# Performance work log

Hardware: AMD Instinct MI355X
Metric: run time of the kernel (lower is better)

The kernel has to match this reference:

```python
import jax, jax.numpy as jnp
import numpy as np

B, V, C, H, W, D = 1, 3, 64, 96, 96, 48


def bilinear_sample(feat, gx, gy):
    """torch F.grid_sample(mode='bilinear', padding_mode='zeros', align_corners=True).
    feat: (B, C, H, W); gx, gy: (B, N) normalized coords in [-1, 1]. Returns (B, C, N)."""
    Bf, Cf, Hf, Wf = feat.shape
    x = (gx + 1.0) * 0.5 * (Wf - 1)
    y = (gy + 1.0) * 0.5 * (Hf - 1)
    x0 = jnp.floor(x)
    y0 = jnp.floor(y)
    wx1 = x - x0
    wy1 = y - y0
    wx0 = 1.0 - wx1
    wy0 = 1.0 - wy1
    flat = feat.reshape(Bf, Cf, Hf * Wf)

    def gather(xi, yi):
        valid = (xi >= 0) & (xi <= Wf - 1) & (yi >= 0) & (yi <= Hf - 1)
        xi_c = jnp.clip(xi, 0, Wf - 1).astype(jnp.int32)
        yi_c = jnp.clip(yi, 0, Hf - 1).astype(jnp.int32)
        idx = (yi_c * Wf + xi_c)[:, None, :]  # (B,1,N), broadcast over C
        return jnp.take_along_axis(flat, idx, axis=2) * valid[:, None, :]

    out = (gather(x0, y0) * (wx0 * wy0)[:, None]
           + gather(x0 + 1, y0) * (wx1 * wy0)[:, None]
           + gather(x0, y0 + 1) * (wx0 * wy1)[:, None]
           + gather(x0 + 1, y0 + 1) * (wx1 * wy1)[:, None])
    return out


def src_grid(proj_mat, depth_values, Hs, Ws):
    """homo_warp grid computation. proj_mat: (B,3,4); depth_values: (B,D).
    Returns normalized gx, gy each of shape (B, D*Hs*Ws)."""
    xs = jnp.arange(Ws, dtype=jnp.float32)
    ys = jnp.arange(Hs, dtype=jnp.float32)
    gx_, gy_ = jnp.meshgrid(xs, ys)  # (Hs, Ws) each
    ref = jnp.stack([gx_.ravel(), gy_.ravel(), jnp.ones(Hs * Ws, jnp.float32)], 0)  # (3, HW)
    R = proj_mat[:, :, :3]
    T = proj_mat[:, :, 3]
    # (B,3,D,HW): R @ p + T / depth
    pts = jnp.einsum('bij,jn->bin', R, ref)[:, :, None, :] + T[:, :, None, None] / depth_values[:, None, :, None]
    xy = pts[:, :2] / pts[:, 2:3]
    gx = xy[:, 0] / ((Ws - 1) / 2.0) - 1.0
    gy = xy[:, 1] / ((Hs - 1) / 2.0) - 1.0
    Bb = proj_mat.shape[0]
    return gx.reshape(Bb, -1), gy.reshape(Bb, -1)


def setup_inputs() -> dict:
    key = jax.random.key(0)
    k1, k2, k3, k4 = jax.random.split(key, 4)
    imgs = jax.random.normal(k1, (B, V, 3, H, W), jnp.float32)
    feats = jax.random.normal(k2, (B, V, C, H, W), jnp.float32)
    # near-identity projections so warped coords land mostly in-range (z ~ 1)
    eye = jnp.broadcast_to(jnp.eye(3, dtype=jnp.float32), (B, V, 3, 3))
    Rn = eye + 0.05 * jax.random.normal(k3, (B, V, 3, 3), jnp.float32)
    Tn = 0.5 * jax.random.normal(jax.random.fold_in(k3, 1), (B, V, 3, 1), jnp.float32)
    proj_mats = jnp.concatenate([Rn, Tn], axis=-1)
    depth_values = 2.0 + 4.0 * jax.random.uniform(k4, (B, D), jnp.float32)
    return {"imgs": imgs, "feats": feats, "proj_mats": proj_mats, "depth_values": depth_values}


def reference(imgs, feats, proj_mats, depth_values):
    Bb, Vv, _, Hh, Ww = imgs.shape
    Cc = feats.shape[2]
    Dd = depth_values.shape[1]
    # ref view volume (broadcast over D)
    ref_volume = jnp.broadcast_to(feats[:, 0][:, :, None], (Bb, Cc, Dd, Hh, Ww))
    volume_sum = ref_volume
    volume_sq_sum = ref_volume ** 2
    mask_sum = jnp.ones((Bb, Dd, Hh, Ww), jnp.float32)  # ref view always in-range
    img_chans = [jnp.broadcast_to(imgs[:, 0][:, :, None], (Bb, 3, Dd, Hh, Ww))]
    for i in range(Vv - 1):  # small fixed number of source views
        gx, gy = src_grid(proj_mats[:, i + 1], depth_values, Hh, Ww)
        wv = bilinear_sample(feats[:, i + 1], gx, gy).reshape(Bb, Cc, Dd, Hh, Ww)
        wi = bilinear_sample(imgs[:, i + 1], gx, gy).reshape(Bb, 3, Dd, Hh, Ww)
        m = ((gx > -1.0) & (gx < 1.0) & (gy > -1.0) & (gy < 1.0)).astype(jnp.float32).reshape(Bb, Dd, Hh, Ww)
        volume_sum = volume_sum + wv
        volume_sq_sum = volume_sq_sum + wv ** 2
        mask_sum = mask_sum + m
        img_chans.append(wi)
    count = 1.0 / mask_sum[:, None]  # (B,1,D,H,W)
    var = volume_sq_sum * count - (volume_sum * count) ** 2  # (B,C,D,H,W)
    img_chans.append(var)
    return jnp.concatenate(img_chans, axis=1)  # (B, 3*V + C, D, H, W)
```

## Files before the change

kernel.cpp:

```cpp
#include <hip/hip_runtime.h>

#define BDIM 256

constexpr int Vv = 3, Cc = 64, Hh = 96, Ww = 96, Dd = 48;
constexpr int HW = Hh * Ww;
constexpr int NPIX = Dd * HW;
constexpr int DHW = Dd * HW;
constexpr int NXCD = 8;
constexpr int WP = Ww + 4;

__device__ __forceinline__ void compute_warp_v(const float* __restrict__ P, float depth,
                                               float xf, float yf,
                                               int offs[4], float wts[4], float& inbf)
{
#pragma clang fp contract(off)
    const float r00 = P[0], r01 = P[1], r02 = P[2],  t0 = P[3];
    const float r10 = P[4], r11 = P[5], r12 = P[6],  t1 = P[7];
    const float r20 = P[8], r21 = P[9], r22 = P[10], t2 = P[11];

    const float px = ((r00 * xf + r01 * yf) + r02) + t0 / depth;
    const float py = ((r10 * xf + r11 * yf) + r12) + t1 / depth;
    const float pz = ((r20 * xf + r21 * yf) + r22) + t2 / depth;

    const float xy0 = px / pz;
    const float xy1 = py / pz;
    const float gx = xy0 / ((float)(Ww - 1) * 0.5f) - 1.0f;
    const float gy = xy1 / ((float)(Hh - 1) * 0.5f) - 1.0f;

    const bool inb = (gx > -1.0f) && (gx < 1.0f) && (gy > -1.0f) && (gy < 1.0f);
    inbf = inb ? 1.0f : 0.0f;

    const float sx = (gx + 1.0f) * 0.5f * (float)(Ww - 1);
    const float sy = (gy + 1.0f) * 0.5f * (float)(Hh - 1);
    const float x0 = floorf(sx), y0 = floorf(sy);
    const float wx1 = sx - x0, wy1 = sy - y0;
    const float wx0 = 1.0f - wx1, wy0 = 1.0f - wy1;

#pragma unroll
    for (int k = 0; k < 4; ++k) {
        const float xi = (k & 1) ? (x0 + 1.0f) : x0;
        const float yi = (k & 2) ? (y0 + 1.0f) : y0;
        const float wk = ((k & 1) ? wx1 : wx0) * ((k & 2) ? wy1 : wy0);
        const bool valid = (xi >= 0.0f) && (xi <= (float)(Ww - 1)) &&
                           (yi >= 0.0f) && (yi <= (float)(Hh - 1));
        const float xc = fminf(fmaxf(xi, 0.0f), (float)(Ww - 1));
        const float yc = fminf(fmaxf(yi, 0.0f), (float)(Hh - 1));
        offs[k] = (int)yc * Ww + (int)xc;
        wts[k] = valid ? wk : 0.0f;
    }
}

__device__ __forceinline__ void compute_warp(const float* __restrict__ proj, float depth,
                                             float xf, float yf,
                                             int offs[2][4], float wts[2][4], float& msum)
{
    msum = 1.0f;
#pragma unroll
    for (int v = 0; v < 2; ++v) {
        float inb;
        compute_warp_v(proj + (v + 1) * 12, depth, xf, yf, offs[v], wts[v], inb);
        msum += inb;
    }
}

__device__ __forceinline__ float var_one(float fr, float a1, float a2, float cnt)
{
    const float s  = fr + a1 + a2;
    const float q  = fr * fr + a1 * a1 + a2 * a2;
    const float sc = s * cnt;
    return q * cnt - sc * sc;
}

__global__ void __launch_bounds__(BDIM) transpose_feats_kernel(const float* __restrict__ feats,
                                                               float* __restrict__ ft)
{
    __shared__ float tile[64][65];
    const int v  = blockIdx.y;
    const int p0 = blockIdx.x * 64;
    const float* src = feats + (size_t)v * Cc * HW;

    const int px = threadIdx.x & 63;
    const int c0 = threadIdx.x >> 6;
#pragma unroll
    for (int c = c0; c < Cc; c += 4)
        tile[c][px] = src[(size_t)c * HW + p0 + px];
    __syncthreads();

    const int cc  = threadIdx.x & 63;
    const int pr0 = threadIdx.x >> 6;
    float* dst = ft + ((size_t)v * HW + p0) * Cc;
#pragma unroll
    for (int p = pr0; p < 64; p += 4)
        dst[p * Cc + cc] = tile[cc][p];
}

__global__ void __launch_bounds__(BDIM) ge_row_kernel(
    const float* __restrict__ imgs, const float* __restrict__ ftr,
    const float* __restrict__ proj, const float* __restrict__ depthv,
    float* __restrict__ out)
{
    __shared__ alignas(16) float s_tile[2][Cc / 2][WP];
    __shared__ alignas(16) int   s_base[2][2][Ww][4];
    __shared__ alignas(16) float s_wt[2][2][Ww][4];
    __shared__ float s_inb[2][2][Ww];

    const int nper = (Hh * (Dd / 2)) / NXCD;
    const int blk  = (blockIdx.x & (NXCD - 1)) * nper + (blockIdx.x >> 3);
    const int h   = blk / (Dd / 2);
    const int dq  = blk - h * (Dd / 2);
    const int d0  = dq * 2;
    const int tid = threadIdx.x;
    const int rowb0 = d0 * HW + h * Ww;

    if (tid < 2 * Ww) {
        const int v = (tid >= Ww) ? 1 : 0;
        const int w = tid - v * Ww;
        const float* ib = imgs + (size_t)(v + 1) * 3 * HW;
#pragma unroll
        for (int dd = 0; dd < 2; ++dd) {
            int offs[4];
            float wts[4];
            float inb;
            compute_warp_v(proj + (v + 1) * 12, depthv[d0 + dd], (float)w, (float)h,
                           offs, wts, inb);
            s_inb[v][dd][w] = inb;
#pragma unroll
            for (int k = 0; k < 4; ++k) {
                s_base[v][dd][w][k] = ((v + 1) * HW + offs[k]) * Cc;
                s_wt[v][dd][w][k]   = wts[k];
            }
#pragma unroll
            for (int c = 0; c < 3; ++c) {
                const float* p = ib + (size_t)c * HW;
                const float acc = wts[0] * p[offs[0]] + wts[1] * p[offs[1]] +
                                  wts[2] * p[offs[2]] + wts[3] * p[offs[3]];
                out[(3 * (v + 1) + c) * DHW + rowb0 + dd * HW + w] = acc;
            }
        }
    }
    if (tid < Ww) {
        const int hw = h * Ww + tid;
#pragma unroll
        for (int c = 0; c < 3; ++c) {
            const float val = imgs[c * HW + hw];
            out[c * DHW + rowb0 + tid]      = val;
            out[c * DHW + rowb0 + HW + tid] = val;
        }
    }
    __syncthreads();

    const int wave = tid >> 6;
    const int lane = tid & 63;
    const int sub  = lane >> 3;
    const int cq   = lane & 7;
    const int c4   = cq << 2;
    const int p0   = wave * (Ww / 4);

#pragma unroll
    for (int hc = 0; hc < 2; ++hc) {
        const int ch0 = hc * (Cc / 2);

        for (int i = 0; i < 3; ++i) {
            const int p = p0 + i * 8 + sub;
            const int4   b00 = *reinterpret_cast<const int4*>(&s_base[0][0][p][0]);
            const int4   b10 = *reinterpret_cast<const int4*>(&s_base[1][0][p][0]);
            const int4   b01 = *reinterpret_cast<const int4*>(&s_base[0][1][p][0]);
            const int4   b11 = *reinterpret_cast<const int4*>(&s_base[1][1][p][0]);
            const float4 w00 = *reinterpret_cast<const float4*>(&s_wt[0][0][p][0]);
            const float4 w10 = *reinterpret_cast<const float4*>(&s_wt[1][0][p][0]);
            const float4 w01 = *reinterpret_cast<const float4*>(&s_wt[0][1][p][0]);
            const float4 w11 = *reinterpret_cast<const float4*>(&s_wt[1][1][p][0]);
            const float cnt0 = 1.0f / (1.0f + s_inb[0][0][p] + s_inb[1][0][p]);
            const float cnt1 = 1.0f / (1.0f + s_inb[0][1][p] + s_inb[1][1][p]);

            const float4 fr = *reinterpret_cast<const float4*>(
                ftr + (size_t)(h * Ww + p) * Cc + ch0 + c4);

            const float4 a00 = *reinterpret_cast<const float4*>(ftr + b00.x + ch0 + c4);
            const float4 a01 = *reinterpret_cast<const float4*>(ftr + b00.y + ch0 + c4);
            const float4 a02 = *reinterpret_cast<const float4*>(ftr + b00.z + ch0 + c4);
            const float4 a03 = *reinterpret_cast<const float4*>(ftr + b00.w + ch0 + c4);
            const float4 a10 = *reinterpret_cast<const float4*>(ftr + b10.x + ch0 + c4);
            const float4 a11 = *reinterpret_cast<const float4*>(ftr + b10.y + ch0 + c4);
            const float4 a12 = *reinterpret_cast<const float4*>(ftr + b10.z + ch0 + c4);
            const float4 a13 = *reinterpret_cast<const float4*>(ftr + b10.w + ch0 + c4);
            const float4 c00 = *reinterpret_cast<const float4*>(ftr + b01.x + ch0 + c4);
            const float4 c01 = *reinterpret_cast<const float4*>(ftr + b01.y + ch0 + c4);
            const float4 c02 = *reinterpret_cast<const float4*>(ftr + b01.z + ch0 + c4);
            const float4 c03 = *reinterpret_cast<const float4*>(ftr + b01.w + ch0 + c4);
            const float4 c10 = *reinterpret_cast<const float4*>(ftr + b11.x + ch0 + c4);
            const float4 c11 = *reinterpret_cast<const float4*>(ftr + b11.y + ch0 + c4);
            const float4 c12 = *reinterpret_cast<const float4*>(ftr + b11.z + ch0 + c4);
            const float4 c13 = *reinterpret_cast<const float4*>(ftr + b11.w + ch0 + c4);

#define VAR_LANE(dd, W0, W1, V0a, V0b, V0c, V0d, V1a, V1b, V1c, V1d, CNT)                 \
            {                                                                              \
                {                                                                          \
                    const float a1 = W0.x * V0a.x + W0.y * V0b.x + W0.z * V0c.x + W0.w * V0d.x; \
                    const float a2 = W1.x * V1a.x + W1.y * V1b.x + W1.z * V1c.x + W1.w * V1d.x; \
                    s_tile[dd][c4 + 0][p] = var_one(fr.x, a1, a2, CNT);                    \
                }                                                                          \
                {                                                                          \
                    const float a1 = W0.x * V0a.y + W0.y * V0b.y + W0.z * V0c.y + W0.w * V0d.y; \
                    const float a2 = W1.x * V1a.y + W1.y * V1b.y + W1.z * V1c.y + W1.w * V1d.y; \
                    s_tile[dd][c4 + 1][p] = var_one(fr.y, a1, a2, CNT);                    \
                }                                                                          \
                {                                                                          \
                    const float a1 = W0.x * V0a.z + W0.y * V0b.z + W0.z * V0c.z + W0.w * V0d.z; \
                    const float a2 = W1.x * V1a.z + W1.y * V1b.z + W1.z * V1c.z + W1.w * V1d.z; \
                    s_tile[dd][c4 + 2][p] = var_one(fr.z, a1, a2, CNT);                    \
                }                                                                          \
                {                                                                          \
                    const float a1 = W0.x * V0a.w + W0.y * V0b.w + W0.z * V0c.w + W0.w * V0d.w; \
                    const float a2 = W1.x * V1a.w + W1.y * V1b.w + W1.z * V1c.w + W1.w * V1d.w; \
                    s_tile[dd][c4 + 3][p] = var_one(fr.w, a1, a2, CNT);                    \
                }                                                                          \
            }

            VAR_LANE(0, w00, w10, a00, a01, a02, a03, a10, a11, a12, a13, cnt0)
            VAR_LANE(1, w01, w11, c00, c01, c02, c03, c10, c11, c12, c13, cnt1)
#undef VAR_LANE
        }
        __syncthreads();

#pragma unroll
        for (int j = 0; j < (2 * (Cc / 2) * (Ww / 4)) / BDIM; ++j) {
            const int idx = tid + j * BDIM;
            const int dd  = idx / ((Cc / 2) * (Ww / 4));
            const int r   = idx - dd * ((Cc / 2) * (Ww / 4));
            const int cc  = r / (Ww / 4);
            const int pq  = r - cc * (Ww / 4);
            const float4 val = *reinterpret_cast<const float4*>(&s_tile[dd][cc][pq * 4]);
            *reinterpret_cast<float4*>(
                &out[(9 + ch0 + cc) * DHW + rowb0 + dd * HW + pq * 4]) = val;
        }
        __syncthreads();
    }
}

__global__ void __launch_bounds__(BDIM) ge_direct_kernel(
    const float* __restrict__ imgs, const float* __restrict__ feats,
    const float* __restrict__ proj, const float* __restrict__ depthv,
    float* __restrict__ out)
{
    const int idx = blockIdx.x * BDIM + threadIdx.x;
    if (idx >= NPIX) return;
    const int w = idx % Ww;
    const int t = idx / Ww;
    const int h = t % Hh;
    const int d = t / Hh;
    const int ohw = h * Ww + w;

    int offs[2][4];
    float wts[2][4];
    float msum;
    compute_warp(proj, depthv[d], (float)w, (float)h, offs, wts, msum);

    const int obase = d * HW + ohw;
#pragma unroll
    for (int c = 0; c < 3; ++c)
        out[c * DHW + obase] = imgs[c * HW + ohw];

#pragma unroll
    for (int v = 0; v < 2; ++v) {
        const float* ib = imgs + (size_t)(v + 1) * 3 * HW;
#pragma unroll
        for (int c = 0; c < 3; ++c) {
            const float* p = ib + (size_t)c * HW;
            const float acc = wts[v][0] * p[offs[v][0]] + wts[v][1] * p[offs[v][1]] +
                              wts[v][2] * p[offs[v][2]] + wts[v][3] * p[offs[v][3]];
            out[(3 * (v + 1) + c) * DHW + obase] = acc;
        }
    }

    const float count = 1.0f / msum;
    const float* f0 = feats;
    const float* f1 = feats + (size_t)Cc * HW;
    const float* f2 = feats + (size_t)2 * Cc * HW;
#pragma unroll 8
    for (int c = 0; c < Cc; ++c) {
        const float fr = f0[(size_t)c * HW + ohw];
        const float* p1 = f1 + (size_t)c * HW;
        const float* p2 = f2 + (size_t)c * HW;
        const float a1 = wts[0][0] * p1[offs[0][0]] + wts[0][1] * p1[offs[0][1]] +
                         wts[0][2] * p1[offs[0][2]] + wts[0][3] * p1[offs[0][3]];
        const float a2 = wts[1][0] * p2[offs[1][0]] + wts[1][1] * p2[offs[1][1]] +
                         wts[1][2] * p2[offs[1][2]] + wts[1][3] * p2[offs[1][3]];
        const float s = fr + a1 + a2;
        const float sq = fr * fr + a1 * a1 + a2 * a2;
        const float sc = s * count;
        out[(3 * Vv + c) * DHW + obase] = sq * count - sc * sc;
    }
}

extern "C" void kernel_launch(void* const* d_in, const int* in_sizes, int n_in,
                              void* d_out, int out_size, void* d_ws, size_t ws_size,
                              hipStream_t stream)
{
    const float* imgs   = (const float*)d_in[0];
    const float* feats  = (const float*)d_in[1];
    const float* proj   = (const float*)d_in[2];
    const float* depthv = (const float*)d_in[3];
    float* out = (float*)d_out;

    const size_t need = (size_t)Vv * HW * Cc * sizeof(float);

    if (ws_size >= need) {
        float* ftr = (float*)d_ws;
        dim3 g1(HW / 64, Vv);
        transpose_feats_kernel<<<g1, BDIM, 0, stream>>>(feats, ftr);
        ge_row_kernel<<<Hh * (Dd / 2), BDIM, 0, stream>>>(imgs, ftr, proj, depthv, out);
    } else {
        const int blocks = (NPIX + BDIM - 1) / BDIM;
        ge_direct_kernel<<<blocks, BDIM, 0, stream>>>(imgs, feats, proj, depthv, out);
    }
}
```

Baseline: 170.1 us.

## Halve shared tile and hold second depth slice in registers to raise occupancy

The transpose tile in LDS is cut from two depth slices to one. The second slice's results are kept in registers and written through the same tile after the first slice is flushed. Launch bounds now ask for 6 blocks per CU, and the reference-image copy moves to the threads left idle by the warp setup. This is meant to lower LDS use and raise occupancy so gather latency is better hidden, at the cost of extra barriers, more register pressure and an extra LDS round trip.

```diff
diff --git a/kernel.cpp b/kernel.cpp
--- a/kernel.cpp
+++ b/kernel.cpp
@@ -94,12 +94,12 @@
         dst[p * Cc + cc] = tile[cc][p];
 }
 
-__global__ void __launch_bounds__(BDIM) ge_row_kernel(
+__global__ void __launch_bounds__(BDIM, 6) ge_row_kernel(
     const float* __restrict__ imgs, const float* __restrict__ ftr,
     const float* __restrict__ proj, const float* __restrict__ depthv,
     float* __restrict__ out)
 {
-    __shared__ alignas(16) float s_tile[2][Cc / 2][WP];
+    __shared__ alignas(16) float s_tile[Cc / 2][WP];
     __shared__ alignas(16) int   s_base[2][2][Ww][4];
     __shared__ alignas(16) float s_wt[2][2][Ww][4];
     __shared__ float s_inb[2][2][Ww];
@@ -137,14 +137,15 @@
                 out[(3 * (v + 1) + c) * DHW + rowb0 + dd * HW + w] = acc;
             }
         }
-    }
-    if (tid < Ww) {
-        const int hw = h * Ww + tid;
-#pragma unroll
-        for (int c = 0; c < 3; ++c) {
-            const float val = imgs[c * HW + hw];
-            out[c * DHW + rowb0 + tid]      = val;
-            out[c * DHW + rowb0 + HW + tid] = val;
+    } else {
+        for (int w = tid - 2 * Ww; w < Ww; w += BDIM - 2 * Ww) {
+            const int hw = h * Ww + w;
+#pragma unroll
+            for (int c = 0; c < 3; ++c) {
+                const float val = imgs[c * HW + hw];
+                out[c * DHW + rowb0 + w]      = val;
+                out[c * DHW + rowb0 + HW + w] = val;
+            }
         }
     }
     __syncthreads();
@@ -159,7 +160,9 @@
 #pragma unroll
     for (int hc = 0; hc < 2; ++hc) {
         const int ch0 = hc * (Cc / 2);
-
+        float4 keep[3];
+
+#pragma unroll
         for (int i = 0; i < 3; ++i) {
             const int p = p0 + i * 8 + sub;
             const int4   b00 = *reinterpret_cast<const int4*>(&s_base[0][0][p][0]);
@@ -193,48 +196,82 @@
             const float4 c12 = *reinterpret_cast<const float4*>(ftr + b11.z + ch0 + c4);
             const float4 c13 = *reinterpret_cast<const float4*>(ftr + b11.w + ch0 + c4);
 
-#define VAR_LANE(dd, W0, W1, V0a, V0b, V0c, V0d, V1a, V1b, V1c, V1d, CNT)                 \
-            {                                                                              \
-                {                                                                          \
-                    const float a1 = W0.x * V0a.x + W0.y * V0b.x + W0.z * V0c.x + W0.w * V0d.x; \
-                    const float a2 = W1.x * V1a.x + W1.y * V1b.x + W1.z * V1c.x + W1.w * V1d.x; \
-                    s_tile[dd][c4 + 0][p] = var_one(fr.x, a1, a2, CNT);                    \
-                }                                                                          \
-                {                                                                          \
-                    const float a1 = W0.x * V0a.y + W0.y * V0b.y + W0.z * V0c.y + W0.w * V0d.y; \
-                    const float a2 = W1.x * V1a.y + W1.y * V1b.y + W1.z * V1c.y + W1.w * V1d.y; \
-                    s_tile[dd][c4 + 1][p] = var_one(fr.y, a1, a2, CNT);                    \
-                }                                                                          \
-                {                                                                          \
-                    const float a1 = W0.x * V0a.z + W0.y * V0b.z + W0.z * V0c.z + W0.w * V0d.z; \
-                    const float a2 = W1.x * V1a.z + W1.y * V1b.z + W1.z * V1c.z + W1.w * V1d.z; \
-                    s_tile[dd][c4 + 2][p] = var_one(fr.z, a1, a2, CNT);                    \
-                }                                                                          \
-                {                                                                          \
-                    const float a1 = W0.x * V0a.w + W0.y * V0b.w + W0.z * V0c.w + W0.w * V0d.w; \
-                    const float a2 = W1.x * V1a.w + W1.y * V1b.w + W1.z * V1c.w + W1.w * V1d.w; \
-                    s_tile[dd][c4 + 3][p] = var_one(fr.w, a1, a2, CNT);                    \
-                }                                                                          \
-            }
-
-            VAR_LANE(0, w00, w10, a00, a01, a02, a03, a10, a11, a12, a13, cnt0)
-            VAR_LANE(1, w01, w11, c00, c01, c02, c03, c10, c11, c12, c13, cnt1)
-#undef VAR_LANE
+            {
+                const float a1 = w00.x * a00.x + w00.y * a01.x + w00.z * a02.x + w00.w * a03.x;
+                const float a2 = w10.x * a10.x + w10.y * a11.x + w10.z * a12.x + w10.w * a13.x;
+                s_tile[c4 + 0][p] = var_one(fr.x, a1, a2, cnt0);
+            }
+            {
+                const float a1 = w00.x * a00.y + w00.y * a01.y + w00.z * a02.y + w00.w * a03.y;
+                const float a2 = w10.x * a10.y + w10.y * a11.y + w10.z * a12.y + w10.w * a13.y;
+                s_tile[c4 + 1][p] = var_one(fr.y, a1, a2, cnt0);
+            }
+            {
+                const float a1 = w00.x * a00.z + w00.y * a01.z + w00.z * a02.z + w00.w * a03.z;
+                const float a2 = w10.x * a10.z + w10.y * a11.z + w10.z * a12.z + w10.w * a13.z;
+                s_tile[c4 + 2][p] = var_one(fr.z, a1, a2, cnt0);
+            }
+            {
+                const float a1 = w00.x * a00.w + w00.y * a01.w + w00.z * a02.w + w00.w * a03.w;
+                const float a2 = w10.x * a10.w + w10.y * a11.w + w10.z * a12.w + w10.w * a13.w;
+                s_tile[c4 + 3][p] = var_one(fr.w, a1, a2, cnt0);
+            }
+            float4 kv;
+            {
+                const float a1 = w01.x * c00.x + w01.y * c01.x + w01.z * c02.x + w01.w * c03.x;
+                const float a2 = w11.x * c10.x + w11.y * c11.x + w11.z * c12.x + w11.w * c13.x;
+                kv.x = var_one(fr.x, a1, a2, cnt1);
+            }
+            {
+                const float a1 = w01.x * c00.y + w01.y * c01.y + w01.z * c02.y + w01.w * c03.y;
+                const float a2 = w11.x * c10.y + w11.y * c11.y + w11.z * c12.y + w11.w * c13.y;
+                kv.y = var_one(fr.y, a1, a2, cnt1);
+            }
+            {
+                const float a1 = w01.x * c00.z + w01.y * c01.z + w01.z * c02.z + w01.w * c03.z;
+                const float a2 = w11.x * c10.z + w11.y * c11.z + w11.z * c12.z + w11.w * c13.z;
+                kv.z = var_one(fr.z, a1, a2, cnt1);
+            }
+            {
+                const float a1 = w01.x * c00.w + w01.y * c01.w + w01.z * c02.w + w01.w * c03.w;
+                const float a2 = w11.x * c10.w + w11.y * c11.w + w11.z * c12.w + w11.w * c13.w;
+                kv.w = var_one(fr.w, a1, a2, cnt1);
+            }
+            keep[i] = kv;
         }
         __syncthreads();
 
 #pragma unroll
-        for (int j = 0; j < (2 * (Cc / 2) * (Ww / 4)) / BDIM; ++j) {
+        for (int j = 0; j < ((Cc / 2) * (Ww / 4)) / BDIM; ++j) {
             const int idx = tid + j * BDIM;
-            const int dd  = idx / ((Cc / 2) * (Ww / 4));
-            const int r   = idx - dd * ((Cc / 2) * (Ww / 4));
-            const int cc  = r / (Ww / 4);
-            const int pq  = r - cc * (Ww / 4);
-            const float4 val = *reinterpret_cast<const float4*>(&s_tile[dd][cc][pq * 4]);
+            const int cc  = idx / (Ww / 4);
+            const int pq  = idx - cc * (Ww / 4);
+            const float4 val = *reinterpret_cast<const float4*>(&s_tile[cc][pq * 4]);
             *reinterpret_cast<float4*>(
-                &out[(9 + ch0 + cc) * DHW + rowb0 + dd * HW + pq * 4]) = val;
+                &out[(9 + ch0 + cc) * DHW + rowb0 + pq * 4]) = val;
         }
         __syncthreads();
+
+#pragma unroll
+        for (int i = 0; i < 3; ++i) {
+            const int p = p0 + i * 8 + sub;
+            s_tile[c4 + 0][p] = keep[i].x;
+            s_tile[c4 + 1][p] = keep[i].y;
+            s_tile[c4 + 2][p] = keep[i].z;
+            s_tile[c4 + 3][p] = keep[i].w;
+        }
+        __syncthreads();
+
+#pragma unroll
+        for (int j = 0; j < ((Cc / 2) * (Ww / 4)) / BDIM; ++j) {
+            const int idx = tid + j * BDIM;
+            const int cc  = idx / (Ww / 4);
+            const int pq  = idx - cc * (Ww / 4);
+            const float4 val = *reinterpret_cast<const float4*>(&s_tile[cc][pq * 4]);
+            *reinterpret_cast<float4*>(
+                &out[(9 + ch0 + cc) * DHW + rowb0 + HW + pq * 4]) = val;
+        }
+        if (hc == 0) __syncthreads();
     }
 }
 
```

Result: no change. 168.3 us, median of 2 (-1.0%).
